# Performance work log

Measured on AMD Instinct MI355X. Metric: run time of the kernel, lower is better.

## Reference

```python
import jax, jax.numpy as jnp
import numpy as np

HIDDEN = 1024


def setup_inputs() -> dict:
    key = jax.random.key(0)
    ks = jax.random.split(key, 8)
    B, S, H = 64, 2048, HIDDEN
    scale = 1.0 / np.sqrt(H)
    return {
        "decoder_hidden": jax.random.normal(ks[0], (B, H), jnp.float32),
        "encoder_outputs": jax.random.normal(ks[1], (B, S, 2 * H), jnp.float32),
        "coverage": jax.random.uniform(ks[2], (B, S), jnp.float32),
        "mask": jnp.ones((B, S), jnp.int32),
        # parameters (nn.Linear weight layout: (out, in); we store transposed for x @ W)
        "W_h": jax.random.normal(ks[3], (2 * H, H), jnp.float32) * scale,
        "W_d": jax.random.normal(ks[4], (H, H), jnp.float32) * scale,
        "W_c": jax.random.normal(ks[5], (1, H), jnp.float32) * scale,
        "v": jax.random.normal(ks[6], (H, 1), jnp.float32) * scale,
    }


def reference(decoder_hidden, encoder_outputs, coverage, mask, W_h, W_d, W_c, v):
    # energy: (B, S, H) = tanh(enc@W_h + dec@W_d broadcast over S + coverage*W_c)
    enc_proj = jnp.einsum("bse,eh->bsh", encoder_outputs, W_h)
    dec_proj = (decoder_hidden @ W_d)[:, None, :]            # (B,1,H)
    cov_proj = coverage[:, :, None] * W_c[0][None, None, :]  # (B,S,H)
    energy = jnp.tanh(enc_proj + dec_proj + cov_proj)
    scores = jnp.einsum("bsh,h->bs", energy, v[:, 0])        # (B,S)
    scores = jnp.where(mask == 0, jnp.float32(-10000.0), scores)
    attn_weights = jax.nn.softmax(scores, axis=1)            # (B,S)
    coverage_new = coverage + attn_weights
    context = jnp.einsum("bs,bse->be", attn_weights, encoder_outputs)  # (B,2H)
    return (context, attn_weights, coverage_new)
```

## Files before the change

kernel.cpp:

```cpp
#include <hip/hip_runtime.h>
#include <hip/hip_bf16.h>
#include <stdint.h>

#define BATCH 64
#define SEQ   2048
#define HID   1024
#define EDIM  2048

#define BM 64
#define BN 512
#define BK 32
#define KSTEPS (EDIM / BK)
#define BS (BATCH * SEQ)

typedef __bf16 bf16x8 __attribute__((ext_vector_type(8)));
typedef float  f32x4a __attribute__((ext_vector_type(4)));

__device__ __forceinline__ unsigned short f2bf(float x) {
    __hip_bfloat16 h = __float2bfloat16(x);
    return __builtin_bit_cast(unsigned short, h);
}

__device__ __forceinline__ uint4 pack8(f32x4a f0, f32x4a f1) {
    uint4 r;
    r.x = (unsigned)f2bf(f0.x) | ((unsigned)f2bf(f0.y) << 16);
    r.y = (unsigned)f2bf(f0.z) | ((unsigned)f2bf(f0.w) << 16);
    r.z = (unsigned)f2bf(f1.x) | ((unsigned)f2bf(f1.y) << 16);
    r.w = (unsigned)f2bf(f1.z) | ((unsigned)f2bf(f1.w) << 16);
    return r;
}

__device__ __forceinline__ f32x4a ntload4(const float* p) {
    return __builtin_nontemporal_load((const f32x4a*)p);
}

__device__ __forceinline__ int a_addr(int row, int g) {
    int slot = g ^ ((row & 3) ^ ((row >> 2) & 3));
    return (row << 6) + (slot << 4);
}

__global__ void wh_transpose_kernel(const float* __restrict__ Wh,
                                    unsigned short* __restrict__ Wt) {
    __shared__ float tile[32][33];
    int bx = blockIdx.x & 63;
    int by = blockIdx.x >> 6;
    int e0 = bx * 32, h0 = by * 32;
    int tx = threadIdx.x & 31, ty = threadIdx.x >> 5;
    #pragma unroll
    for (int i = 0; i < 4; ++i)
        tile[ty + 8 * i][tx] = Wh[(size_t)(e0 + ty + 8 * i) * HID + h0 + tx];
    __syncthreads();
    if (ty < 4) {
        uint4 wv;
        unsigned short* ws = (unsigned short*)&wv;
        #pragma unroll
        for (int j = 0; j < 8; ++j) ws[j] = f2bf(tile[ty * 8 + j][tx]);
        *(uint4*)&Wt[(size_t)((e0 >> 3) + ty) * 8192 + (size_t)(h0 + tx) * 8] = wv;
    }
}

__global__ void dec_proj_kernel(const float* __restrict__ dec,
                                const float* __restrict__ Wd,
                                float* __restrict__ dp) {
    int gid = blockIdx.x * 256 + threadIdx.x;
    int b = gid >> 10, h = gid & 1023;
    const float* dr = dec + b * HID;
    float acc = 0.f;
    #pragma unroll 4
    for (int k = 0; k < HID; ++k) acc = fmaf(dr[k], Wd[(size_t)k * HID + h], acc);
    dp[gid] = acc;
}

#define MFMA16(a, bfv, c) __builtin_amdgcn_mfma_f32_16x16x32_bf16(a, bfv, c, 0, 0, 0)

__global__ __launch_bounds__(512, 4) void scores_kernel(
    const float* __restrict__ enc, const float* __restrict__ cov,
    const unsigned short* __restrict__ Wt, const float* __restrict__ dp,
    const float* __restrict__ Wc, const float* __restrict__ vv,
    float* __restrict__ spart_out)
{
    __shared__ char Al[2][4096];
    __shared__ float cov_s[BM];
    __shared__ float sred[BM][8];

    const int tid  = threadIdx.x;
    const int lane = tid & 63;
    const int wid  = tid >> 6;
    const int c15  = lane & 15;
    const int g4   = lane >> 4;

    const int bid  = blockIdx.x;
    const int half = bid & 1;
    const int m    = bid >> 1;
    const int b    = m >> 5;
    const int s0   = (m & 31) * BM;

    const float* Abase = enc + (size_t)(b * SEQ + s0) * EDIM;
    const int arow = tid >> 2;
    const int ag   = tid & 3;

    const unsigned short* bptr =
        Wt + (size_t)g4 * 8192 + (size_t)(half * BN + wid * 64 + c15) * 8;

    f32x4a acc[4][4];
    #pragma unroll
    for (int mi = 0; mi < 4; ++mi)
        #pragma unroll
        for (int nj = 0; nj < 4; ++nj)
            #pragma unroll
            for (int r = 0; r < 4; ++r) acc[mi][nj][r] = 0.f;

    if (tid < BM) cov_s[tid] = cov[b * SEQ + s0 + tid];

    if (tid < 256) {
        const float* ap = Abase + (size_t)arow * EDIM + ag * 8;
        *(uint4*)(Al[0] + a_addr(arow, ag)) = pack8(ntload4(ap), ntload4(ap + 4));
    }
    __syncthreads();

    for (int kk = 0; kk < KSTEPS; ++kk) {
        const int cur = kk & 1, nxt = cur ^ 1;

        bf16x8 bfr[4];
        #pragma unroll
        for (int nj = 0; nj < 4; ++nj)
            bfr[nj] = *(const bf16x8*)(bptr + nj * 128);
        bptr += 4 * 8192;

        f32x4a a0n, a1n;
        if (kk + 1 < KSTEPS && tid < 256) {
            const float* ap = Abase + (size_t)arow * EDIM + (kk + 1) * BK + ag * 8;
            a0n = ntload4(ap); a1n = ntload4(ap + 4);
        }

        bf16x8 afr[4];
        #pragma unroll
        for (int mi = 0; mi < 4; ++mi)
            afr[mi] = *(const bf16x8*)(Al[cur] + a_addr(mi * 16 + c15, g4));

        #pragma unroll
        for (int mi = 0; mi < 4; ++mi)
            #pragma unroll
            for (int nj = 0; nj < 4; ++nj)
                acc[mi][nj] = MFMA16(afr[mi], bfr[nj], acc[mi][nj]);

        if (kk + 1 < KSTEPS && tid < 256)
            *(uint4*)(Al[nxt] + a_addr(arow, ag)) = pack8(a0n, a1n);
        __syncthreads();
    }

    float spart[4][4];
    #pragma unroll
    for (int mi = 0; mi < 4; ++mi)
        #pragma unroll
        for (int r = 0; r < 4; ++r) spart[mi][r] = 0.f;

    #pragma unroll
    for (int nj = 0; nj < 4; ++nj) {
        const int h = half * BN + wid * 64 + nj * 16 + c15;
        const float dv  = dp[b * HID + h];
        const float wcv = Wc[h];
        const float vvv = vv[h];
        #pragma unroll
        for (int mi = 0; mi < 4; ++mi) {
            #pragma unroll
            for (int r = 0; r < 4; ++r) {
                const int row = mi * 16 + g4 * 4 + r;
                float pre = acc[mi][nj][r] + dv + cov_s[row] * wcv;
                float pc = fminf(pre, 20.0f);
                float e2 = __expf(2.0f * pc);
                spart[mi][r] = fmaf((e2 - 1.0f) / (e2 + 1.0f), vvv, spart[mi][r]);
            }
        }
    }
    #pragma unroll
    for (int mi = 0; mi < 4; ++mi) {
        #pragma unroll
        for (int r = 0; r < 4; ++r) {
            float x = spart[mi][r];
            x += __shfl_xor(x, 1);
            x += __shfl_xor(x, 2);
            x += __shfl_xor(x, 4);
            x += __shfl_xor(x, 8);
            if (c15 == 0) sred[mi * 16 + g4 * 4 + r][wid] = x;
        }
    }
    __syncthreads();
    if (tid < BM) {
        float s = 0.f;
        #pragma unroll
        for (int w = 0; w < 8; ++w) s += sred[tid][w];
        spart_out[(size_t)half * BS + b * SEQ + s0 + tid] = s;
    }
}

__global__ void softmax_kernel(const float* __restrict__ spart,
                               const int* __restrict__ mask,
                               const float* __restrict__ cov,
                               float* __restrict__ out)
{
    __shared__ float red[8];
    int b = blockIdx.x, tid = threadIdx.x;
    float vals[8];
    float mx = -1e30f;
    #pragma unroll
    for (int i = 0; i < 8; ++i) {
        int s = tid + i * 256;
        float sc = spart[b * SEQ + s] + spart[BS + b * SEQ + s];
        sc = (mask[b * SEQ + s] == 0) ? -10000.0f : sc;
        vals[i] = sc;
        mx = fmaxf(mx, sc);
    }
    for (int m = 1; m < 64; m <<= 1) mx = fmaxf(mx, __shfl_xor(mx, m));
    if ((tid & 63) == 0) red[tid >> 6] = mx;
    __syncthreads();
    mx = fmaxf(fmaxf(red[0], red[1]), fmaxf(red[2], red[3]));
    float sum = 0.f;
    #pragma unroll
    for (int i = 0; i < 8; ++i) { vals[i] = __expf(vals[i] - mx); sum += vals[i]; }
    for (int m = 1; m < 64; m <<= 1) sum += __shfl_xor(sum, m);
    if ((tid & 63) == 0) red[4 + (tid >> 6)] = sum;
    __syncthreads();
    sum = red[4] + red[5] + red[6] + red[7];
    float inv = 1.0f / sum;
    float* attn = out + BATCH * EDIM;
    float* covn = attn + BATCH * SEQ;
    #pragma unroll
    for (int i = 0; i < 8; ++i) {
        int s = tid + i * 256;
        float w = vals[i] * inv;
        attn[b * SEQ + s] = w;
        covn[b * SEQ + s] = cov[b * SEQ + s] + w;
    }
}

__global__ void context_partial_kernel(const float* __restrict__ enc,
                                       const float* __restrict__ attn,
                                       float* __restrict__ cpart)
{
    __shared__ float w_s[512];
    int bid = blockIdx.x;
    int sc = bid & 3;
    int e0 = ((bid >> 2) & 7) * 256;
    int b  = bid >> 5;
    int tid = threadIdx.x;
    w_s[tid] = attn[b * SEQ + sc * 512 + tid];
    w_s[tid + 256] = attn[b * SEQ + sc * 512 + 256 + tid];
    __syncthreads();
    const float* ep = enc + ((size_t)b * SEQ + sc * 512) * EDIM + e0 + tid;
    float acc = 0.f;
    #pragma unroll 8
    for (int s = 0; s < 512; ++s)
        acc = fmaf(w_s[s], __builtin_nontemporal_load(ep + (size_t)s * EDIM), acc);
    cpart[((size_t)sc * BATCH + b) * EDIM + e0 + tid] = acc;
}

__global__ void ctx_reduce_kernel(const float* __restrict__ cpart,
                                  float* __restrict__ ctx)
{
    int idx = blockIdx.x * 256 + threadIdx.x;
    ctx[idx] = cpart[idx] + cpart[BATCH * EDIM + idx] +
               cpart[2 * BATCH * EDIM + idx] + cpart[3 * BATCH * EDIM + idx];
}

extern "C" void kernel_launch(void* const* d_in, const int* in_sizes, int n_in,
                              void* d_out, int out_size, void* d_ws, size_t ws_size,
                              hipStream_t stream) {
    const float* dec  = (const float*)d_in[0];
    const float* enc  = (const float*)d_in[1];
    const float* cov  = (const float*)d_in[2];
    const int*   mask = (const int*)d_in[3];
    const float* Wh   = (const float*)d_in[4];
    const float* Wd   = (const float*)d_in[5];
    const float* Wc   = (const float*)d_in[6];
    const float* v    = (const float*)d_in[7];
    float* out = (float*)d_out;

    unsigned short* Wt = (unsigned short*)d_ws;
    float* dp    = (float*)((char*)d_ws + (size_t)HID * EDIM * 2);
    float* spart = dp + BATCH * HID;
    float* cpart = spart + 2 * BS;

    wh_transpose_kernel<<<dim3(64 * 32), dim3(256), 0, stream>>>(Wh, Wt);
    dec_proj_kernel<<<dim3(BATCH * HID / 256), dim3(256), 0, stream>>>(dec, Wd, dp);
    scores_kernel<<<dim3((BS / BM) * 2), dim3(512), 0, stream>>>(
        enc, cov, Wt, dp, Wc, v, spart);
    softmax_kernel<<<dim3(BATCH), dim3(256), 0, stream>>>(spart, mask, cov, out);
    context_partial_kernel<<<dim3(BATCH * 8 * 4), dim3(256), 0, stream>>>(
        enc, out + BATCH * EDIM, cpart);
    ctx_reduce_kernel<<<dim3(BATCH * EDIM / 256), dim3(256), 0, stream>>>(cpart, out);
}
```

Baseline: 1.049 ms.

## Software-pipeline the scores GEMM main loop with register double-buffered B fragments

Restructures the scores GEMM K-loop so W_h fragments for the next step are loaded into a second register buffer while the current step's MFMAs run, and the encoder A tile is prefetched two steps ahead. All 512 threads now share the A loads (4 floats each instead of 8 floats on half the threads), and a new XOR swizzle is used for LDS writes and reads. The loop is unrolled by two with explicit s_setprio around the MFMAs, an lgkmcnt wait, and a raw s_barrier plus sched_barrier. This aims to hide global-load latency behind MFMAs, at the cost of more registers and reliance on hand-placed scheduling barriers.

```diff
diff --git a/kernel.cpp b/kernel.cpp
--- a/kernel.cpp
+++ b/kernel.cpp
@@ -21,12 +21,10 @@
     return __builtin_bit_cast(unsigned short, h);
 }
 
-__device__ __forceinline__ uint4 pack8(f32x4a f0, f32x4a f1) {
-    uint4 r;
-    r.x = (unsigned)f2bf(f0.x) | ((unsigned)f2bf(f0.y) << 16);
-    r.y = (unsigned)f2bf(f0.z) | ((unsigned)f2bf(f0.w) << 16);
-    r.z = (unsigned)f2bf(f1.x) | ((unsigned)f2bf(f1.y) << 16);
-    r.w = (unsigned)f2bf(f1.z) | ((unsigned)f2bf(f1.w) << 16);
+__device__ __forceinline__ uint2 pack4(f32x4a f) {
+    uint2 r;
+    r.x = (unsigned)f2bf(f.x) | ((unsigned)f2bf(f.y) << 16);
+    r.y = (unsigned)f2bf(f.z) | ((unsigned)f2bf(f.w) << 16);
     return r;
 }
 
@@ -34,9 +32,11 @@
     return __builtin_nontemporal_load((const f32x4a*)p);
 }
 
-__device__ __forceinline__ int a_addr(int row, int g) {
-    int slot = g ^ ((row & 3) ^ ((row >> 2) & 3));
-    return (row << 6) + (slot << 4);
+__device__ __forceinline__ int a_waddr(int row, int c) {
+    return (row << 6) + ((c ^ (row & 6)) << 3);
+}
+__device__ __forceinline__ int a_raddr(int row, int g) {
+    return (row << 6) + ((g ^ ((row >> 1) & 3)) << 4);
 }
 
 __global__ void wh_transpose_kernel(const float* __restrict__ Wh,
@@ -73,6 +73,30 @@
 
 #define MFMA16(a, bfv, c) __builtin_amdgcn_mfma_f32_16x16x32_bf16(a, bfv, c, 0, 0, 0)
 
+#define KSTEP(kk, BCUR, BNXT, CURBUF, NXTBUF)                                   \
+  {                                                                             \
+    if ((kk) + 1 < KSTEPS) {                                                    \
+      const unsigned short* bs = bptr + (size_t)((kk) + 1) * 32768;             \
+      _Pragma("unroll")                                                         \
+      for (int nj = 0; nj < 4; ++nj)                                            \
+        BNXT[nj] = *(const bf16x8*)(bs + nj * 128);                             \
+    }                                                                           \
+    __builtin_amdgcn_s_setprio(1);                                              \
+    _Pragma("unroll")                                                           \
+    for (int mi = 0; mi < 4; ++mi) {                                            \
+      bf16x8 afr = *(const bf16x8*)(CURBUF + a_raddr(mi * 16 + c15, g4));       \
+      _Pragma("unroll")                                                         \
+      for (int nj = 0; nj < 4; ++nj)                                            \
+        acc[mi][nj] = MFMA16(afr, BCUR[nj], acc[mi][nj]);                       \
+    }                                                                           \
+    __builtin_amdgcn_s_setprio(0);                                              \
+    if ((kk) + 1 < KSTEPS) *(uint2*)(NXTBUF + wb) = pack4(aL);                  \
+    if ((kk) + 2 < KSTEPS) aL = ntload4(ap0 + ((kk) + 2) * BK);                 \
+    asm volatile("s_waitcnt lgkmcnt(0)" ::: "memory");                          \
+    __builtin_amdgcn_s_barrier();                                               \
+    __builtin_amdgcn_sched_barrier(0);                                          \
+  }
+
 __global__ __launch_bounds__(512, 4) void scores_kernel(
     const float* __restrict__ enc, const float* __restrict__ cov,
     const unsigned short* __restrict__ Wt, const float* __restrict__ dp,
@@ -96,8 +120,10 @@
     const int s0   = (m & 31) * BM;
 
     const float* Abase = enc + (size_t)(b * SEQ + s0) * EDIM;
-    const int arow = tid >> 2;
-    const int ag   = tid & 3;
+    const int arow = tid >> 3;
+    const int ac   = tid & 7;
+    const float* ap0 = Abase + (size_t)arow * EDIM + ac * 4;
+    const int wb = a_waddr(arow, ac);
 
     const unsigned short* bptr =
         Wt + (size_t)g4 * 8192 + (size_t)(half * BN + wid * 64 + c15) * 8;
@@ -112,41 +138,20 @@
 
     if (tid < BM) cov_s[tid] = cov[b * SEQ + s0 + tid];
 
-    if (tid < 256) {
-        const float* ap = Abase + (size_t)arow * EDIM + ag * 8;
-        *(uint4*)(Al[0] + a_addr(arow, ag)) = pack8(ntload4(ap), ntload4(ap + 4));
-    }
-    __syncthreads();
-
-    for (int kk = 0; kk < KSTEPS; ++kk) {
-        const int cur = kk & 1, nxt = cur ^ 1;
-
-        bf16x8 bfr[4];
-        #pragma unroll
-        for (int nj = 0; nj < 4; ++nj)
-            bfr[nj] = *(const bf16x8*)(bptr + nj * 128);
-        bptr += 4 * 8192;
-
-        f32x4a a0n, a1n;
-        if (kk + 1 < KSTEPS && tid < 256) {
-            const float* ap = Abase + (size_t)arow * EDIM + (kk + 1) * BK + ag * 8;
-            a0n = ntload4(ap); a1n = ntload4(ap + 4);
-        }
-
-        bf16x8 afr[4];
-        #pragma unroll
-        for (int mi = 0; mi < 4; ++mi)
-            afr[mi] = *(const bf16x8*)(Al[cur] + a_addr(mi * 16 + c15, g4));
-
-        #pragma unroll
-        for (int mi = 0; mi < 4; ++mi)
-            #pragma unroll
-            for (int nj = 0; nj < 4; ++nj)
-                acc[mi][nj] = MFMA16(afr[mi], bfr[nj], acc[mi][nj]);
-
-        if (kk + 1 < KSTEPS && tid < 256)
-            *(uint4*)(Al[nxt] + a_addr(arow, ag)) = pack8(a0n, a1n);
-        __syncthreads();
+    bf16x8 bA[4], bB[4];
+    f32x4a aL = ntload4(ap0);
+    #pragma unroll
+    for (int nj = 0; nj < 4; ++nj)
+        bA[nj] = *(const bf16x8*)(bptr + nj * 128);
+    *(uint2*)(Al[0] + wb) = pack4(aL);
+    aL = ntload4(ap0 + BK);
+    asm volatile("s_waitcnt lgkmcnt(0)" ::: "memory");
+    __builtin_amdgcn_s_barrier();
+    __builtin_amdgcn_sched_barrier(0);
+
+    for (int kk2 = 0; kk2 < KSTEPS; kk2 += 2) {
+        KSTEP(kk2,     bA, bB, Al[0], Al[1]);
+        KSTEP(kk2 + 1, bB, bA, Al[1], Al[0]);
     }
 
     float spart[4][4];
```

After: 985.3 us, median of 3. -6.0%, faster.
